# Performance work log

Measured on AMD Instinct MI355X. Metric: run time of the kernel, lower is better.

Reference implementation:

```python
import jax, jax.numpy as jnp
import numpy as np

N_OSC = 256
BATCH = 1024
DT = 0.1
STEPS = 10


def setup_inputs() -> dict:
    key = jax.random.key(0)
    k_theta, k_K, k_omega = jax.random.split(key, 3)
    theta_init = jax.random.normal(k_theta, (BATCH, N_OSC), dtype=jnp.float32)
    K0 = jax.random.normal(k_K, (N_OSC, N_OSC), dtype=jnp.float32) * 0.1
    K = (K0 + K0.T) / 2  # symmetric coupling matrix, as in torch init
    omega = jax.random.normal(k_omega, (N_OSC,), dtype=jnp.float32) * 0.1
    K_global = jnp.float32(0.5)
    return {"theta_init": theta_init, "K": K, "omega": omega, "K_global": K_global}


def reference(theta_init, K, omega, K_global):
    n = K.shape[0]

    def step(theta, _):
        # diff[b, i, j] = theta[b, j] - theta[b, i]
        diff = theta[..., None, :] - theta[..., :, None]
        coupling_sum = jnp.sum(K * jnp.sin(diff), axis=-1)  # (batch, n)
        dtheta = omega + (K_global / n) * coupling_sum
        theta_new = theta + DT * dtheta
        # wrap to (-pi, pi]
        theta_new = jnp.arctan2(jnp.sin(theta_new), jnp.cos(theta_new))
        return theta_new, None

    theta, _ = jax.lax.scan(step, theta_init, None, length=STEPS)
    cos_mean = jnp.cos(theta).mean(axis=-1)
    sin_mean = jnp.sin(theta).mean(axis=-1)
    coherence = jnp.sqrt(cos_mean ** 2 + sin_mean ** 2)
    return theta, coherence
```

## Files before the change

kernel.cpp:

```cpp
#include <hip/hip_runtime.h>
#include <math.h>


typedef __attribute__((ext_vector_type(8))) short short8;
typedef __attribute__((ext_vector_type(4))) float f32x4;

constexpr int N       = 256;
constexpr int RB      = 16;
constexpr int STEPS   = 10;
constexpr int WAVES   = 8;
constexpr int THREADS = WAVES * 64;
constexpr float DT    = 0.1f;
constexpr float TWO_PI     = 6.28318530717958648f;
constexpr float INV_TWO_PI = 0.15915494309189535f;

__device__ __forceinline__ unsigned short f2bf(float f) {
    unsigned u = __float_as_uint(f);
    return (unsigned short)((u + 0x8000u) >> 16);
}

__global__ __launch_bounds__(THREADS, 2)
void kuramoto_mfma(const float* __restrict__ theta0,
                   const float* __restrict__ Kmat,
                   const float* __restrict__ omega,
                   const float* __restrict__ kglob,
                   float* __restrict__ theta_out,
                   float* __restrict__ coh_out)
{
    __shared__ __align__(16) unsigned short SC[2][2][RB][N];
    __shared__ float redS[RB][WAVES];
    __shared__ float redC[RB][WAVES];

    const int tid  = threadIdx.x;
    const int wv   = tid >> 6;
    const int lane = tid & 63;
    const int q    = lane >> 4;
    const int l15  = lane & 15;
    const int b0   = blockIdx.x * RB;

    const float kgn = kglob[0] * (1.0f / (float)N);

    short8 kf[2][8];
#pragma unroll
    for (int t = 0; t < 2; ++t) {
        const int n = 32 * wv + 16 * t + l15;
        const float* kr = Kmat + (size_t)n * N + 8 * q;
#pragma unroll
        for (int c = 0; c < 8; ++c) {
            float4 lo = *(const float4*)(kr + 32 * c);
            float4 hi = *(const float4*)(kr + 32 * c + 4);
            short8 v;
            v[0] = (short)f2bf(lo.x); v[1] = (short)f2bf(lo.y);
            v[2] = (short)f2bf(lo.z); v[3] = (short)f2bf(lo.w);
            v[4] = (short)f2bf(hi.x); v[5] = (short)f2bf(hi.y);
            v[6] = (short)f2bf(hi.z); v[7] = (short)f2bf(hi.w);
            kf[t][c] = v;
        }
    }

    float thv[2][4], om[2];
#pragma unroll
    for (int t = 0; t < 2; ++t) {
        const int col = 32 * wv + 16 * t + l15;
        om[t] = omega[col];
#pragma unroll
        for (int r = 0; r < 4; ++r)
            thv[t][r] = theta0[(size_t)(b0 + 4 * q + r) * N + col];
    }

    float sv[2][4], cv[2][4];

    for (int s = 0; s < STEPS; ++s) {
        const int buf = s & 1;
#pragma unroll
        for (int t = 0; t < 2; ++t) {
            const int j = 32 * wv + 16 * t + l15;
            const int g = j >> 3, o = j & 7;
#pragma unroll
            for (int r = 0; r < 4; ++r) {
                __sincosf(thv[t][r], &sv[t][r], &cv[t][r]);
                const int row  = 4 * q + r;
                const int phys = ((g ^ (row & 7)) << 3) + o;
                SC[buf][0][row][phys] = f2bf(sv[t][r]);
                SC[buf][1][row][phys] = f2bf(cv[t][r]);
            }
        }
        __syncthreads();

        f32x4 aS[2], aC[2];
#pragma unroll
        for (int t = 0; t < 2; ++t) {
            aS[t] = (f32x4){0.f, 0.f, 0.f, 0.f};
            aC[t] = (f32x4){0.f, 0.f, 0.f, 0.f};
        }
#pragma unroll
        for (int c = 0; c < 8; ++c) {
            const int phys = ((4 * c + q) ^ (l15 & 7)) << 3;
            short8 As = *(const short8*)&SC[buf][0][l15][phys];
            short8 Ac = *(const short8*)&SC[buf][1][l15][phys];
#pragma unroll
            for (int t = 0; t < 2; ++t) {
                aS[t] = __builtin_amdgcn_mfma_f32_16x16x32_bf16(As, kf[t][c], aS[t], 0, 0, 0);
                aC[t] = __builtin_amdgcn_mfma_f32_16x16x32_bf16(Ac, kf[t][c], aC[t], 0, 0, 0);
            }
        }

#pragma unroll
        for (int t = 0; t < 2; ++t) {
#pragma unroll
            for (int r = 0; r < 4; ++r) {
                float coup = cv[t][r] * aS[t][r] - sv[t][r] * aC[t][r];
                thv[t][r] = fmaf(DT, fmaf(kgn, coup, om[t]), thv[t][r]);
            }
        }
    }

    float sumS[4] = {0.f, 0.f, 0.f, 0.f};
    float sumC[4] = {0.f, 0.f, 0.f, 0.f};
#pragma unroll
    for (int t = 0; t < 2; ++t) {
        const int col = 32 * wv + 16 * t + l15;
#pragma unroll
        for (int r = 0; r < 4; ++r) {
            float th = thv[t][r];
            float s0, c0;
            __sincosf(th, &s0, &c0);
            float w = fmaf(-TWO_PI, rintf(th * INV_TWO_PI), th);
            theta_out[(size_t)(b0 + 4 * q + r) * N + col] = w;
            sumS[r] += s0;
            sumC[r] += c0;
        }
    }
#pragma unroll
    for (int r = 0; r < 4; ++r) {
#pragma unroll
        for (int off = 1; off <= 8; off <<= 1) {
            sumS[r] += __shfl_xor(sumS[r], off, 64);
            sumC[r] += __shfl_xor(sumC[r], off, 64);
        }
    }
    if (l15 == 0) {
#pragma unroll
        for (int r = 0; r < 4; ++r) {
            redS[4 * q + r][wv] = sumS[r];
            redC[4 * q + r][wv] = sumC[r];
        }
    }
    __syncthreads();
    if (tid < RB) {
        float S = 0.f, C = 0.f;
#pragma unroll
        for (int k = 0; k < WAVES; ++k) { S += redS[tid][k]; C += redC[tid][k]; }
        float sm = S * (1.0f / (float)N);
        float cm = C * (1.0f / (float)N);
        coh_out[b0 + tid] = sqrtf(sm * sm + cm * cm);
    }
}

extern "C" void kernel_launch(void* const* d_in, const int* in_sizes, int n_in,
                              void* d_out, int out_size, void* d_ws, size_t ws_size,
                              hipStream_t stream) {
    const float* theta0 = (const float*)d_in[0];
    const float* Kmat   = (const float*)d_in[1];
    const float* omega  = (const float*)d_in[2];
    const float* kglob  = (const float*)d_in[3];

    float* theta_out = (float*)d_out;
    float* coh_out   = theta_out + 1024 * N;

    kuramoto_mfma<<<dim3(1024 / RB), dim3(THREADS), 0, stream>>>(
        theta0, Kmat, omega, kglob, theta_out, coh_out);
}
```

Before: 76.07 us.

## Switch coupling matmul from bf16 to fp8 MFMA with transposed operand layout

Replaces the bf16 MFMA coupling product with fp8 MFMA, converting K and the per-step sin/cos values to packed fp8. The operands are swapped so each lane owns a batch row and four consecutive oscillators, which lets sin and cos be packed into a single 8-byte LDS store and read back with one 16-byte load per chunk, using a new XOR swizzle. The goal is to halve LDS traffic and register footprint for K and to use the faster fp8 MFMA path. The cost is much lower precision for the coupling matrix and trig values, which may push results past the accuracy tolerance.

```diff
diff --git a/kernel.cpp b/kernel.cpp
--- a/kernel.cpp
+++ b/kernel.cpp
@@ -2,7 +2,6 @@
 #include <math.h>
 
 
-typedef __attribute__((ext_vector_type(8))) short short8;
 typedef __attribute__((ext_vector_type(4))) float f32x4;
 
 constexpr int N       = 256;
@@ -14,22 +13,16 @@
 constexpr float TWO_PI     = 6.28318530717958648f;
 constexpr float INV_TWO_PI = 0.15915494309189535f;
 
-__device__ __forceinline__ unsigned short f2bf(float f) {
-    unsigned u = __float_as_uint(f);
-    return (unsigned short)((u + 0x8000u) >> 16);
-}
-
 __global__ __launch_bounds__(THREADS, 2)
-void kuramoto_mfma(const float* __restrict__ theta0,
-                   const float* __restrict__ Kmat,
-                   const float* __restrict__ omega,
-                   const float* __restrict__ kglob,
-                   float* __restrict__ theta_out,
-                   float* __restrict__ coh_out)
+void kuramoto_fp8(const float* __restrict__ theta0,
+                  const float* __restrict__ Kmat,
+                  const float* __restrict__ omega,
+                  const float* __restrict__ kglob,
+                  float* __restrict__ theta_out,
+                  float* __restrict__ coh_out)
 {
-    __shared__ __align__(16) unsigned short SC[2][2][RB][N];
-    __shared__ float redS[RB][WAVES];
-    __shared__ float redC[RB][WAVES];
+    __shared__ __align__(16) unsigned char SC[2][RB][512];
+    __shared__ float redS[RB][WAVES], redC[RB][WAVES];
 
     const int tid  = threadIdx.x;
     const int wv   = tid >> 6;
@@ -38,35 +31,34 @@
     const int l15  = lane & 15;
     const int b0   = blockIdx.x * RB;
 
-    const float kgn = kglob[0] * (1.0f / (float)N);
+    const float kgn = kglob[0] * (1.0f / 256.0f);
 
-    short8 kf[2][8];
+    long kf[2][8];
 #pragma unroll
     for (int t = 0; t < 2; ++t) {
-        const int n = 32 * wv + 16 * t + l15;
-        const float* kr = Kmat + (size_t)n * N + 8 * q;
+        const int i = 32 * wv + 16 * t + l15;
+        const float* kr = Kmat + (size_t)i * N + 8 * q;
 #pragma unroll
         for (int c = 0; c < 8; ++c) {
             float4 lo = *(const float4*)(kr + 32 * c);
             float4 hi = *(const float4*)(kr + 32 * c + 4);
-            short8 v;
-            v[0] = (short)f2bf(lo.x); v[1] = (short)f2bf(lo.y);
-            v[2] = (short)f2bf(lo.z); v[3] = (short)f2bf(lo.w);
-            v[4] = (short)f2bf(hi.x); v[5] = (short)f2bf(hi.y);
-            v[6] = (short)f2bf(hi.z); v[7] = (short)f2bf(hi.w);
-            kf[t][c] = v;
+            int w0 = __builtin_amdgcn_cvt_pk_fp8_f32(lo.x, lo.y, 0, false);
+            w0     = __builtin_amdgcn_cvt_pk_fp8_f32(lo.z, lo.w, w0, true);
+            int w1 = __builtin_amdgcn_cvt_pk_fp8_f32(hi.x, hi.y, 0, false);
+            w1     = __builtin_amdgcn_cvt_pk_fp8_f32(hi.z, hi.w, w1, true);
+            kf[t][c] = (long)(unsigned)w0 | ((long)w1 << 32);
         }
     }
 
-    float thv[2][4], om[2];
+    float thv[2][4], om[2][4];
 #pragma unroll
-    for (int t = 0; t < 2; ++t) {
-        const int col = 32 * wv + 16 * t + l15;
-        om[t] = omega[col];
+    for (int t = 0; t < 2; ++t)
 #pragma unroll
-        for (int r = 0; r < 4; ++r)
-            thv[t][r] = theta0[(size_t)(b0 + 4 * q + r) * N + col];
-    }
+        for (int r = 0; r < 4; ++r) {
+            const int i = 32 * wv + 16 * t + 4 * q + r;
+            om[t][r]  = omega[i];
+            thv[t][r] = theta0[(size_t)(b0 + l15) * N + i];
+        }
 
     float sv[2][4], cv[2][4];
 
@@ -74,16 +66,17 @@
         const int buf = s & 1;
 #pragma unroll
         for (int t = 0; t < 2; ++t) {
-            const int j = 32 * wv + 16 * t + l15;
-            const int g = j >> 3, o = j & 7;
 #pragma unroll
-            for (int r = 0; r < 4; ++r) {
+            for (int r = 0; r < 4; ++r)
                 __sincosf(thv[t][r], &sv[t][r], &cv[t][r]);
-                const int row  = 4 * q + r;
-                const int phys = ((g ^ (row & 7)) << 3) + o;
-                SC[buf][0][row][phys] = f2bf(sv[t][r]);
-                SC[buf][1][row][phys] = f2bf(cv[t][r]);
-            }
+            int spk = __builtin_amdgcn_cvt_pk_fp8_f32(sv[t][0], sv[t][1], 0, false);
+            spk     = __builtin_amdgcn_cvt_pk_fp8_f32(sv[t][2], sv[t][3], spk, true);
+            int cpk = __builtin_amdgcn_cvt_pk_fp8_f32(cv[t][0], cv[t][1], 0, false);
+            cpk     = __builtin_amdgcn_cvt_pk_fp8_f32(cv[t][2], cv[t][3], cpk, true);
+            const int g = 8 * wv + 4 * t + q;
+            const int u = (g >> 1) ^ l15;
+            int2 val; val.x = spk; val.y = cpk;
+            *(int2*)&SC[buf][l15][16 * u + 8 * (g & 1)] = val;
         }
         __syncthreads();
 
@@ -95,64 +88,48 @@
         }
 #pragma unroll
         for (int c = 0; c < 8; ++c) {
-            const int phys = ((4 * c + q) ^ (l15 & 7)) << 3;
-            short8 As = *(const short8*)&SC[buf][0][l15][phys];
-            short8 Ac = *(const short8*)&SC[buf][1][l15][phys];
+            const int uu = (4 * c + q) ^ l15;
+            int4 vvv = *(const int4*)&SC[buf][l15][16 * uu];
+            long Bs = (long)(unsigned)vvv.x | ((long)vvv.z << 32);
+            long Bc = (long)(unsigned)vvv.y | ((long)vvv.w << 32);
 #pragma unroll
             for (int t = 0; t < 2; ++t) {
-                aS[t] = __builtin_amdgcn_mfma_f32_16x16x32_bf16(As, kf[t][c], aS[t], 0, 0, 0);
-                aC[t] = __builtin_amdgcn_mfma_f32_16x16x32_bf16(Ac, kf[t][c], aC[t], 0, 0, 0);
+                aS[t] = __builtin_amdgcn_mfma_f32_16x16x32_fp8_fp8(kf[t][c], Bs, aS[t], 0, 0, 0);
+                aC[t] = __builtin_amdgcn_mfma_f32_16x16x32_fp8_fp8(kf[t][c], Bc, aC[t], 0, 0, 0);
             }
         }
 
 #pragma unroll
-        for (int t = 0; t < 2; ++t) {
+        for (int t = 0; t < 2; ++t)
 #pragma unroll
             for (int r = 0; r < 4; ++r) {
                 float coup = cv[t][r] * aS[t][r] - sv[t][r] * aC[t][r];
-                thv[t][r] = fmaf(DT, fmaf(kgn, coup, om[t]), thv[t][r]);
+                thv[t][r] = fmaf(DT, fmaf(kgn, coup, om[t][r]), thv[t][r]);
             }
-        }
     }
 
-    float sumS[4] = {0.f, 0.f, 0.f, 0.f};
-    float sumC[4] = {0.f, 0.f, 0.f, 0.f};
+    float ps = 0.f, pc = 0.f;
 #pragma unroll
-    for (int t = 0; t < 2; ++t) {
-        const int col = 32 * wv + 16 * t + l15;
+    for (int t = 0; t < 2; ++t)
 #pragma unroll
         for (int r = 0; r < 4; ++r) {
             float th = thv[t][r];
             float s0, c0;
             __sincosf(th, &s0, &c0);
             float w = fmaf(-TWO_PI, rintf(th * INV_TWO_PI), th);
-            theta_out[(size_t)(b0 + 4 * q + r) * N + col] = w;
-            sumS[r] += s0;
-            sumC[r] += c0;
+            theta_out[(size_t)(b0 + l15) * N + 32 * wv + 16 * t + 4 * q + r] = w;
+            ps += s0; pc += c0;
         }
-    }
-#pragma unroll
-    for (int r = 0; r < 4; ++r) {
-#pragma unroll
-        for (int off = 1; off <= 8; off <<= 1) {
-            sumS[r] += __shfl_xor(sumS[r], off, 64);
-            sumC[r] += __shfl_xor(sumC[r], off, 64);
-        }
-    }
-    if (l15 == 0) {
-#pragma unroll
-        for (int r = 0; r < 4; ++r) {
-            redS[4 * q + r][wv] = sumS[r];
-            redC[4 * q + r][wv] = sumC[r];
-        }
-    }
+    ps += __shfl_xor(ps, 16, 64);  pc += __shfl_xor(pc, 16, 64);
+    ps += __shfl_xor(ps, 32, 64);  pc += __shfl_xor(pc, 32, 64);
+    if (q == 0) { redS[l15][wv] = ps; redC[l15][wv] = pc; }
     __syncthreads();
     if (tid < RB) {
         float S = 0.f, C = 0.f;
 #pragma unroll
         for (int k = 0; k < WAVES; ++k) { S += redS[tid][k]; C += redC[tid][k]; }
-        float sm = S * (1.0f / (float)N);
-        float cm = C * (1.0f / (float)N);
+        float sm = S * (1.0f / 256.0f);
+        float cm = C * (1.0f / 256.0f);
         coh_out[b0 + tid] = sqrtf(sm * sm + cm * cm);
     }
 }
@@ -168,6 +145,6 @@
     float* theta_out = (float*)d_out;
     float* coh_out   = theta_out + 1024 * N;
 
-    kuramoto_mfma<<<dim3(1024 / RB), dim3(THREADS), 0, stream>>>(
+    kuramoto_fp8<<<dim3(1024 / RB), dim3(THREADS), 0, stream>>>(
         theta0, Kmat, omega, kglob, theta_out, coh_out);
 }
```

After: 75.19 us. Within noise of the previous version (-1.2%).
